# Optimization experiments

Measured on AMD Instinct MI355X. Metric: run time of the kernel, lower is better.

Reference implementation:

```python
import jax, jax.numpy as jnp
import numpy as np

N_USERS = 100000
N_ITEMS = 200000
N_NODES = N_USERS + N_ITEMS
EMB_DIM = 64
N_EDGES = 4000000
N_LAYERS = 2
BATCH = 8192
EMB_REG = 2.5e-5


def setup_inputs() -> dict:
    key = jax.random.key(0)
    k = jax.random.split(key, 7)
    return {
        "user_emb": jax.random.normal(k[0], (N_USERS, EMB_DIM), jnp.float32) * 0.1,
        "item_emb": jax.random.normal(k[1], (N_ITEMS, EMB_DIM), jnp.float32) * 0.1,
        "all_h": jax.random.randint(k[2], (N_EDGES,), 0, N_NODES, jnp.int64 if jax.config.jax_enable_x64 else jnp.int32),
        "all_t": jax.random.randint(k[3], (N_EDGES,), 0, N_NODES, jnp.int64 if jax.config.jax_enable_x64 else jnp.int32),
        "users": jax.random.randint(k[4], (BATCH,), 0, N_USERS),
        "pos_items": jax.random.randint(k[5], (BATCH,), 0, N_ITEMS),
        "neg_items": jax.random.randint(k[6], (BATCH,), 0, N_ITEMS),
    }


def _spmm(h, t, vals, x):
    # out[h] += vals * x[t]  over all edges; [N_NODES, D]
    return jax.ops.segment_sum(vals[:, None] * x[t], h, num_segments=N_NODES)


def reference(user_emb, item_emb, all_h, all_t, users, pos_items, neg_items):
    # symmetric normalization G = D^{-1/2} A D^{-1/2} on the edge list
    deg = jax.ops.segment_sum(jnp.ones((all_h.shape[0],), user_emb.dtype), all_h,
                              num_segments=N_NODES)
    dinv = jnp.where(deg > 0, deg ** -0.5, 0.0)
    g_vals = dinv[all_h] * dinv[all_t]

    # inference1: n_layers of SpMM with residual; sum over all layer outputs
    # (dropout p=0 on the main branch in the source -> identity)
    emb = jnp.concatenate([user_emb, item_emb], axis=0)  # [N, D]
    acc = emb
    for _ in range(N_LAYERS):
        emb = _spmm(all_h, all_t, g_vals, emb) + emb
        acc = acc + emb
    ua, ia = acc[:N_USERS], acc[N_USERS:]

    # BPR loss on the batch
    u = ua[users]
    pos = ia[pos_items]
    neg = ia[neg_items]
    pos_scores = jnp.sum(u * pos, axis=1)
    neg_scores = jnp.sum(u * neg, axis=1)
    mf_loss = jnp.mean(jax.nn.softplus(neg_scores - pos_scores))

    # embedding L2 regularization on the pre-propagation embeddings
    u_pre = user_emb[users]
    pos_pre = item_emb[pos_items]
    neg_pre = item_emb[neg_items]
    emb_loss = EMB_REG * (jnp.sum(u_pre ** 2) + jnp.sum(pos_pre ** 2)
                          + jnp.sum(neg_pre ** 2))
    return (mf_loss, emb_loss)
```

## Files before the change

### kernel.cpp

```cpp
#include <hip/hip_runtime.h>
#include <math.h>

#define N_USERS 100000
#define N_ITEMS 200000
#define N_NODES 300000
#define EMB_DIM 64
#define N_EDGES 4000000
#define BATCH   8192
#define EMB_REG 2.5e-05f

#define BUCK_SH 9
#define BN      512
#define NBUCK   586
#define BSLOT   7424
#define EPB     8192
#define EPT     32
#define NBLK_A  489
#define PACK_SH 19
#define SCORE_BLOCKS (BATCH / 4)
#define BLOCKS_PER_RANGE 9375

typedef unsigned short u16;
typedef unsigned int   u32;
typedef unsigned char  u8;
typedef __attribute__((ext_vector_type(8))) u16 u16x8;
typedef __attribute__((ext_vector_type(2))) float f32x2;

__device__ __forceinline__ float bf2f(u16 x) {
    u32 u = ((u32)x) << 16;
    return __builtin_bit_cast(float, u);
}
__device__ __forceinline__ u16 f2bf(float f) {
    u32 u = __builtin_bit_cast(u32, f);
    return (u16)((u + 0x7FFFu + ((u >> 16) & 1u)) >> 16);
}

__global__ void k_init(int* __restrict__ bcur) {
    int i = blockIdx.x * blockDim.x + threadIdx.x;
    if (i < NBUCK) bcur[i] = i * BSLOT;
}

__global__ void k_mark(const int* __restrict__ users, const int* __restrict__ pos,
                       const int* __restrict__ neg, u8* __restrict__ flags) {
    int i = blockIdx.x * blockDim.x + threadIdx.x;
    if (i < BATCH) {
        flags[users[i]] = 1;
        flags[N_USERS + pos[i]] = 1;
        flags[N_USERS + neg[i]] = 1;
    }
}

__global__ __launch_bounds__(256) void kA(const int* __restrict__ hh,
                                          const int* __restrict__ tt,
                                          int* __restrict__ bcur, int* __restrict__ gp) {
    __shared__ int sh_cnt[NBUCK];
    __shared__ int sh_base[NBUCK];
    int tid = threadIdx.x;
    for (int j = tid; j < NBUCK; j += 256) sh_cnt[j] = 0;
    __syncthreads();
    int cbase = blockIdx.x * EPB;
    int clen  = min(EPB, N_EDGES - cbase);
    int pk[EPT], bk[EPT];
    #pragma unroll
    for (int j = 0; j < EPT; ++j) {
        int i = j * 256 + tid;
        bk[j] = -1;
        if (i < clen) {
            int h = hh[cbase + i];
            int t = tt[cbase + i];
            int b = h >> BUCK_SH;
            bk[j] = b;
            pk[j] = ((h & (BN - 1)) << PACK_SH) | t;
            atomicAdd(&sh_cnt[b], 1);
        }
    }
    __syncthreads();
    for (int j = tid; j < NBUCK; j += 256) {
        int c = sh_cnt[j];
        sh_base[j] = c ? atomicAdd(&bcur[j], c) : 0;
        sh_cnt[j] = 0;
    }
    __syncthreads();
    #pragma unroll
    for (int j = 0; j < EPT; ++j) {
        if (bk[j] >= 0) {
            int r = atomicAdd(&sh_cnt[bk[j]], 1);
            gp[sh_base[bk[j]] + r] = pk[j];
        }
    }
}

__global__ __launch_bounds__(256) void kB(const int* __restrict__ bcur,
                                          int* __restrict__ gp,
                                          int2* __restrict__ sde, float* __restrict__ dinv,
                                          const float* __restrict__ uemb,
                                          const float* __restrict__ iemb,
                                          u8* __restrict__ e0s8) {
    __shared__ int   ncnt[BN];
    __shared__ int   noff[BN];
    __shared__ float sdv[BN];
    __shared__ int   slots[BSLOT];
    int b = blockIdx.x;
    int node0 = b << BUCK_SH;
    int nn = min(BN, N_NODES - node0);
    int base = b * BSLOT;
    int count = bcur[b] - base;
    int tid = threadIdx.x;
    for (int j = tid; j < BN; j += 256) ncnt[j] = 0;
    __syncthreads();
    for (int i = tid; i < count; i += 256)
        atomicAdd(&ncnt[gp[base + i] >> PACK_SH], 1);
    __syncthreads();
    if (tid < 64) {
        int lane = tid, carry = 0;
        #pragma unroll
        for (int b0 = 0; b0 < BN; b0 += 64) {
            int idx = b0 + lane;
            int v = ncnt[idx];
            int incl = v;
            #pragma unroll
            for (int d = 1; d < 64; d <<= 1) {
                int u = __shfl_up(incl, d, 64);
                if (lane >= d) incl += u;
            }
            noff[idx] = carry + incl - v;
            carry += __shfl(incl, 63, 64);
        }
    }
    __syncthreads();
    for (int j = tid; j < nn; j += 256) {
        int c = ncnt[j];
        float dv = c > 0 ? rsqrtf((float)c) : 0.0f;
        sde[node0 + j]  = make_int2(base + noff[j], c);
        dinv[node0 + j] = dv;
        sdv[j] = dv;
    }
    __syncthreads();
    for (int j = tid; j < BN; j += 256) ncnt[j] = noff[j];
    __syncthreads();
    for (int i = tid; i < count; i += 256) {
        int p = gp[base + i];
        int r = atomicAdd(&ncnt[p >> PACK_SH], 1);
        slots[r] = p & ((1 << PACK_SH) - 1);
    }
    __syncthreads();
    for (int i = tid; i < count; i += 256)
        gp[base + i] = slots[i];
    for (int i = tid; i < nn * 8; i += 256) {
        int j = i >> 3;
        float sc = sdv[j];
        int gnode = node0 + j;
        size_t ebase = (size_t)gnode * EMB_DIM + (size_t)(i & 7) * 8;
        const size_t UELEMS = (size_t)N_USERS * EMB_DIM;
        const float* src = (ebase < UELEMS) ? uemb + ebase : iemb + (ebase - UELEMS);
        float4 a  = ((const float4*)src)[0];
        float4 c4 = ((const float4*)src)[1];
        u32 w0 = __builtin_amdgcn_cvt_pk_fp8_f32(sc * a.x,  sc * a.y,  0,  false);
        w0 = __builtin_amdgcn_cvt_pk_fp8_f32(sc * a.z,  sc * a.w,  w0, true);
        u32 w1 = __builtin_amdgcn_cvt_pk_fp8_f32(sc * c4.x, sc * c4.y, 0,  false);
        w1 = __builtin_amdgcn_cvt_pk_fp8_f32(sc * c4.z, sc * c4.w, w1, true);
        uint2 o; o.x = w0; o.y = w1;
        ((uint2*)e0s8)[(size_t)gnode * 8 + (i & 7)] = o;
    }
}

__global__ void k_spmm1(const int2* __restrict__ sde,
                        const int* __restrict__ et,
                        const float* __restrict__ dinv,
                        const u8* __restrict__ src8,
                        const float* __restrict__ uemb, const float* __restrict__ iemb,
                        const u8* __restrict__ flags,
                        u16* __restrict__ dstb, u8* __restrict__ dst8) {
    int b = blockIdx.x;
    int node = ((b & 7) * BLOCKS_PER_RANGE + (b >> 3)) * 4 + (threadIdx.x >> 6);
    int lane = threadIdx.x & 63;
    int grp = lane >> 3;
    int sl  = lane & 7;
    int2 se = sde[node];
    int s = se.x, ne = se.y;
    float dh = dinv[node];
    int ets = (lane < ne) ? et[s + lane] : 0;
    float acc[8] = {0.f, 0.f, 0.f, 0.f, 0.f, 0.f, 0.f, 0.f};
    int lim = ne < 64 ? ne : 64;
    for (int j = grp; j < lim; j += 8) {
        int t = __shfl(ets, j, 64);
        uint2 d8 = ((const uint2*)(src8 + (size_t)t * EMB_DIM))[sl];
        f32x2 p0 = __builtin_amdgcn_cvt_pk_f32_fp8(d8.x, false);
        f32x2 p1 = __builtin_amdgcn_cvt_pk_f32_fp8(d8.x, true);
        f32x2 p2 = __builtin_amdgcn_cvt_pk_f32_fp8(d8.y, false);
        f32x2 p3 = __builtin_amdgcn_cvt_pk_f32_fp8(d8.y, true);
        acc[0] += p0.x; acc[1] += p0.y;
        acc[2] += p1.x; acc[3] += p1.y;
        acc[4] += p2.x; acc[5] += p2.y;
        acc[6] += p3.x; acc[7] += p3.y;
    }
    for (int i = s + 64 + grp; i < s + ne; i += 8) {
        int t = et[i];
        uint2 d8 = ((const uint2*)(src8 + (size_t)t * EMB_DIM))[sl];
        f32x2 p0 = __builtin_amdgcn_cvt_pk_f32_fp8(d8.x, false);
        f32x2 p1 = __builtin_amdgcn_cvt_pk_f32_fp8(d8.x, true);
        f32x2 p2 = __builtin_amdgcn_cvt_pk_f32_fp8(d8.y, false);
        f32x2 p3 = __builtin_amdgcn_cvt_pk_f32_fp8(d8.y, true);
        acc[0] += p0.x; acc[1] += p0.y;
        acc[2] += p1.x; acc[3] += p1.y;
        acc[4] += p2.x; acc[5] += p2.y;
        acc[6] += p3.x; acc[7] += p3.y;
    }
    #pragma unroll
    for (int m = 8; m <= 32; m <<= 1) {
        #pragma unroll
        for (int k = 0; k < 8; ++k)
            acc[k] += __shfl_xor(acc[k], m, 64);
    }
    if (grp == 0) {
        const float* srow = (node < N_USERS)
            ? uemb + (size_t)node * EMB_DIM
            : iemb + (size_t)(node - N_USERS) * EMB_DIM;
        float4 a = ((const float4*)srow)[sl * 2];
        float4 c = ((const float4*)srow)[sl * 2 + 1];
        float v[8];
        v[0] = dh * acc[0] + a.x; v[1] = dh * acc[1] + a.y;
        v[2] = dh * acc[2] + a.z; v[3] = dh * acc[3] + a.w;
        v[4] = dh * acc[4] + c.x; v[5] = dh * acc[5] + c.y;
        v[6] = dh * acc[6] + c.z; v[7] = dh * acc[7] + c.w;
        u32 w0 = __builtin_amdgcn_cvt_pk_fp8_f32(dh * v[0], dh * v[1], 0, false);
        w0 = __builtin_amdgcn_cvt_pk_fp8_f32(dh * v[2], dh * v[3], w0, true);
        u32 w1 = __builtin_amdgcn_cvt_pk_fp8_f32(dh * v[4], dh * v[5], 0, false);
        w1 = __builtin_amdgcn_cvt_pk_fp8_f32(dh * v[6], dh * v[7], w1, true);
        uint2 ow; ow.x = w0; ow.y = w1;
        ((uint2*)(dst8 + (size_t)node * EMB_DIM))[sl] = ow;
        if (flags[node]) {
            u16x8 o;
            o.s0 = f2bf(v[0]); o.s1 = f2bf(v[1]); o.s2 = f2bf(v[2]); o.s3 = f2bf(v[3]);
            o.s4 = f2bf(v[4]); o.s5 = f2bf(v[5]); o.s6 = f2bf(v[6]); o.s7 = f2bf(v[7]);
            ((u16x8*)(dstb + (size_t)node * EMB_DIM))[sl] = o;
        }
    }
}

__global__ void k_score(const int* __restrict__ users, const int* __restrict__ pos,
                        const int* __restrict__ neg,
                        const float* __restrict__ uemb, const float* __restrict__ iemb,
                        const u16* __restrict__ emb1b, const u8* __restrict__ emb1s8,
                        const int2* __restrict__ sde, const int* __restrict__ et,
                        const float* __restrict__ dinv,
                        float* __restrict__ pmf, float* __restrict__ psq) {
    __shared__ float smf[4], ssq[4];
    int gid = blockIdx.x * blockDim.x + threadIdx.x;
    int b = gid >> 6;
    int d = gid & 63;
    int w = threadIdx.x >> 6;
    int u  = users[b];
    int pi = pos[b];
    int ni = neg[b];
    int nodes[3];
    nodes[0] = u; nodes[1] = N_USERS + pi; nodes[2] = N_USERS + ni;
    float pre[3];
    pre[0] = uemb[(size_t)u * EMB_DIM + d];
    pre[1] = iemb[(size_t)pi * EMB_DIM + d];
    pre[2] = iemb[(size_t)ni * EMB_DIM + d];
    int s0[3], ne[3], ets[3];
    float dv[3];
    #pragma unroll
    for (int k = 0; k < 3; ++k) {
        int v = nodes[k];
        int2 se = sde[v];
        s0[k] = se.x; ne[k] = se.y;
        dv[k] = dinv[v];
        ets[k] = (d < ne[k]) ? et[se.x + d] : 0;
    }
    float a[3];
    #pragma unroll
    for (int k = 0; k < 3; ++k) {
        float ac = 0.f;
        int lim = ne[k] < 64 ? ne[k] : 64;
        for (int j = 0; j < lim; ++j) {
            int t = __shfl(ets[k], j, 64);
            u32 byte = emb1s8[(size_t)t * EMB_DIM + d];
            ac += __builtin_amdgcn_cvt_f32_fp8(byte, 0);
        }
        for (int i = s0[k] + 64; i < s0[k] + ne[k]; ++i) {
            int t = et[i];
            u32 byte = emb1s8[(size_t)t * EMB_DIM + d];
            ac += __builtin_amdgcn_cvt_f32_fp8(byte, 0);
        }
        a[k] = pre[k] + 2.0f * bf2f(emb1b[(size_t)nodes[k] * EMB_DIM + d]) + dv[k] * ac;
    }
    float ps = a[0] * a[1];
    float ns = a[0] * a[2];
    float sq = pre[0] * pre[0] + pre[1] * pre[1] + pre[2] * pre[2];
    #pragma unroll
    for (int off2 = 32; off2 > 0; off2 >>= 1) {
        ps += __shfl_down(ps, off2, 64);
        ns += __shfl_down(ns, off2, 64);
        sq += __shfl_down(sq, off2, 64);
    }
    if (d == 0) {
        float x  = ns - ps;
        smf[w] = fmaxf(x, 0.0f) + log1pf(expf(-fabsf(x)));
        ssq[w] = sq;
    }
    __syncthreads();
    if (threadIdx.x == 0) {
        pmf[blockIdx.x] = smf[0] + smf[1] + smf[2] + smf[3];
        psq[blockIdx.x] = ssq[0] + ssq[1] + ssq[2] + ssq[3];
    }
}

__global__ void k_final(const float* __restrict__ pmf, const float* __restrict__ psq,
                        float* __restrict__ out) {
    __shared__ float smf[4], ssq[4];
    int tid = threadIdx.x;
    float mf = 0.f, sq = 0.f;
    #pragma unroll
    for (int i = 0; i < SCORE_BLOCKS / 256; ++i) {
        mf += pmf[tid + i * 256];
        sq += psq[tid + i * 256];
    }
    #pragma unroll
    for (int off2 = 32; off2 > 0; off2 >>= 1) {
        mf += __shfl_down(mf, off2, 64);
        sq += __shfl_down(sq, off2, 64);
    }
    if ((tid & 63) == 0) { smf[tid >> 6] = mf; ssq[tid >> 6] = sq; }
    __syncthreads();
    if (tid == 0) {
        out[0] = (smf[0] + smf[1] + smf[2] + smf[3]) * (1.0f / BATCH);
        out[1] = EMB_REG * (ssq[0] + ssq[1] + ssq[2] + ssq[3]);
    }
}

extern "C" void kernel_launch(void* const* d_in, const int* in_sizes, int n_in,
                              void* d_out, int out_size, void* d_ws, size_t ws_size,
                              hipStream_t stream) {
    const float* uemb  = (const float*)d_in[0];
    const float* iemb  = (const float*)d_in[1];
    const int*   all_h = (const int*)d_in[2];
    const int*   all_t = (const int*)d_in[3];
    const int*   users = (const int*)d_in[4];
    const int*   pos   = (const int*)d_in[5];
    const int*   neg   = (const int*)d_in[6];
    float* out = (float*)d_out;

    int*   ws     = (int*)d_ws;
    float* dinv   = (float*)ws;
    int2*  sde    = (int2*)(ws + 300032);
    int*   bcur   = ws + 900096;
    u8*    flags  = (u8*)(ws + 901120);
    float* pmf    = (float*)(ws + 976128);
    float* psq    = (float*)(ws + 978176);
    int*   gp     = ws + 980224;
    u8*    e0s8   = (u8*)(ws + 5330688);
    u8*    emb1s8 = (u8*)(ws + 10130688);
    u16*   emb1b  = (u16*)(ws + 14930688);

    hipMemsetAsync(flags, 0, N_NODES, stream);

    k_init <<<3, 256, 0, stream>>>(bcur);
    k_mark <<<BATCH / 256, 256, 0, stream>>>(users, pos, neg, flags);
    kA     <<<NBLK_A, 256, 0, stream>>>(all_h, all_t, bcur, gp);
    kB     <<<NBUCK, 256, 0, stream>>>(bcur, gp, sde, dinv, uemb, iemb, e0s8);

    k_spmm1<<<N_NODES / 4, 256, 0, stream>>>(sde, gp, dinv, e0s8, uemb, iemb,
                                             flags, emb1b, emb1s8);

    k_score<<<SCORE_BLOCKS, 256, 0, stream>>>(users, pos, neg, uemb, iemb,
                                              emb1b, emb1s8, sde, gp, dinv, pmf, psq);
    k_final<<<1, 256, 0, stream>>>(pmf, psq, out);
}
```

Before: 340.9 us.

## Map one 8-lane group per node in SpMM and compute dinv inline

The first-layer SpMM kernel now assigns each node to an 8-lane subgroup (8 nodes per wavefront, 32 per block) instead of a full 64-lane wavefront, which removes the cross-lane shuffle reduction and avoids idle lanes on low-degree nodes. Edge indices are loaded 8 at a time per group and broadcast by shuffle, and the loop runs to the wave-wide maximum degree. The degree normalisation is recomputed as rsqrt of the edge count instead of being loaded from the dinv array. Divergence between nodes of different degree inside a wave can leave lanes idle, and the interleaved block-to-node mapping is dropped.

```diff
diff --git a/kernel.cpp b/kernel.cpp
--- a/kernel.cpp
+++ b/kernel.cpp
@@ -18,7 +18,6 @@
 #define NBLK_A  489
 #define PACK_SH 19
 #define SCORE_BLOCKS (BATCH / 4)
-#define BLOCKS_PER_RANGE 9375
 
 typedef unsigned short u16;
 typedef unsigned int   u32;
@@ -164,77 +163,65 @@
     }
 }
 
-__global__ void k_spmm1(const int2* __restrict__ sde,
+__global__ __launch_bounds__(256) void k_spmm1(const int2* __restrict__ sde,
                         const int* __restrict__ et,
-                        const float* __restrict__ dinv,
                         const u8* __restrict__ src8,
                         const float* __restrict__ uemb, const float* __restrict__ iemb,
                         const u8* __restrict__ flags,
                         u16* __restrict__ dstb, u8* __restrict__ dst8) {
-    int b = blockIdx.x;
-    int node = ((b & 7) * BLOCKS_PER_RANGE + (b >> 3)) * 4 + (threadIdx.x >> 6);
     int lane = threadIdx.x & 63;
-    int grp = lane >> 3;
-    int sl  = lane & 7;
+    int g    = lane >> 3;
+    int sl   = lane & 7;
+    int gb   = lane & 56;
+    int node = blockIdx.x * 32 + ((threadIdx.x >> 6) << 3) + g;
     int2 se = sde[node];
     int s = se.x, ne = se.y;
-    float dh = dinv[node];
-    int ets = (lane < ne) ? et[s + lane] : 0;
+    float dh = ne > 0 ? rsqrtf((float)ne) : 0.0f;
+    int mx = ne;
+    mx = max(mx, __shfl_xor(mx, 8, 64));
+    mx = max(mx, __shfl_xor(mx, 16, 64));
+    mx = max(mx, __shfl_xor(mx, 32, 64));
     float acc[8] = {0.f, 0.f, 0.f, 0.f, 0.f, 0.f, 0.f, 0.f};
-    int lim = ne < 64 ? ne : 64;
-    for (int j = grp; j < lim; j += 8) {
-        int t = __shfl(ets, j, 64);
-        uint2 d8 = ((const uint2*)(src8 + (size_t)t * EMB_DIM))[sl];
-        f32x2 p0 = __builtin_amdgcn_cvt_pk_f32_fp8(d8.x, false);
-        f32x2 p1 = __builtin_amdgcn_cvt_pk_f32_fp8(d8.x, true);
-        f32x2 p2 = __builtin_amdgcn_cvt_pk_f32_fp8(d8.y, false);
-        f32x2 p3 = __builtin_amdgcn_cvt_pk_f32_fp8(d8.y, true);
-        acc[0] += p0.x; acc[1] += p0.y;
-        acc[2] += p1.x; acc[3] += p1.y;
-        acc[4] += p2.x; acc[5] += p2.y;
-        acc[6] += p3.x; acc[7] += p3.y;
-    }
-    for (int i = s + 64 + grp; i < s + ne; i += 8) {
-        int t = et[i];
-        uint2 d8 = ((const uint2*)(src8 + (size_t)t * EMB_DIM))[sl];
-        f32x2 p0 = __builtin_amdgcn_cvt_pk_f32_fp8(d8.x, false);
-        f32x2 p1 = __builtin_amdgcn_cvt_pk_f32_fp8(d8.x, true);
-        f32x2 p2 = __builtin_amdgcn_cvt_pk_f32_fp8(d8.y, false);
-        f32x2 p3 = __builtin_amdgcn_cvt_pk_f32_fp8(d8.y, true);
-        acc[0] += p0.x; acc[1] += p0.y;
-        acc[2] += p1.x; acc[3] += p1.y;
-        acc[4] += p2.x; acc[5] += p2.y;
-        acc[6] += p3.x; acc[7] += p3.y;
-    }
-    #pragma unroll
-    for (int m = 8; m <= 32; m <<= 1) {
+    for (int j0 = 0; j0 < mx; j0 += 8) {
+        int idx = j0 + sl;
+        int ets = (idx < ne) ? et[s + idx] : 0;
         #pragma unroll
-        for (int k = 0; k < 8; ++k)
-            acc[k] += __shfl_xor(acc[k], m, 64);
-    }
-    if (grp == 0) {
-        const float* srow = (node < N_USERS)
-            ? uemb + (size_t)node * EMB_DIM
-            : iemb + (size_t)(node - N_USERS) * EMB_DIM;
-        float4 a = ((const float4*)srow)[sl * 2];
-        float4 c = ((const float4*)srow)[sl * 2 + 1];
-        float v[8];
-        v[0] = dh * acc[0] + a.x; v[1] = dh * acc[1] + a.y;
-        v[2] = dh * acc[2] + a.z; v[3] = dh * acc[3] + a.w;
-        v[4] = dh * acc[4] + c.x; v[5] = dh * acc[5] + c.y;
-        v[6] = dh * acc[6] + c.z; v[7] = dh * acc[7] + c.w;
-        u32 w0 = __builtin_amdgcn_cvt_pk_fp8_f32(dh * v[0], dh * v[1], 0, false);
-        w0 = __builtin_amdgcn_cvt_pk_fp8_f32(dh * v[2], dh * v[3], w0, true);
-        u32 w1 = __builtin_amdgcn_cvt_pk_fp8_f32(dh * v[4], dh * v[5], 0, false);
-        w1 = __builtin_amdgcn_cvt_pk_fp8_f32(dh * v[6], dh * v[7], w1, true);
-        uint2 ow; ow.x = w0; ow.y = w1;
-        ((uint2*)(dst8 + (size_t)node * EMB_DIM))[sl] = ow;
-        if (flags[node]) {
-            u16x8 o;
-            o.s0 = f2bf(v[0]); o.s1 = f2bf(v[1]); o.s2 = f2bf(v[2]); o.s3 = f2bf(v[3]);
-            o.s4 = f2bf(v[4]); o.s5 = f2bf(v[5]); o.s6 = f2bf(v[6]); o.s7 = f2bf(v[7]);
-            ((u16x8*)(dstb + (size_t)node * EMB_DIM))[sl] = o;
-        }
+        for (int jj = 0; jj < 8; ++jj) {
+            if (j0 + jj < ne) {
+                int t = __shfl(ets, gb | jj, 64);
+                uint2 d8 = ((const uint2*)(src8 + (size_t)t * EMB_DIM))[sl];
+                f32x2 p0 = __builtin_amdgcn_cvt_pk_f32_fp8(d8.x, false);
+                f32x2 p1 = __builtin_amdgcn_cvt_pk_f32_fp8(d8.x, true);
+                f32x2 p2 = __builtin_amdgcn_cvt_pk_f32_fp8(d8.y, false);
+                f32x2 p3 = __builtin_amdgcn_cvt_pk_f32_fp8(d8.y, true);
+                acc[0] += p0.x; acc[1] += p0.y;
+                acc[2] += p1.x; acc[3] += p1.y;
+                acc[4] += p2.x; acc[5] += p2.y;
+                acc[6] += p3.x; acc[7] += p3.y;
+            }
+        }
+    }
+    const float* srow = (node < N_USERS)
+        ? uemb + (size_t)node * EMB_DIM
+        : iemb + (size_t)(node - N_USERS) * EMB_DIM;
+    float4 a = ((const float4*)srow)[sl * 2];
+    float4 c = ((const float4*)srow)[sl * 2 + 1];
+    float v[8];
+    v[0] = dh * acc[0] + a.x; v[1] = dh * acc[1] + a.y;
+    v[2] = dh * acc[2] + a.z; v[3] = dh * acc[3] + a.w;
+    v[4] = dh * acc[4] + c.x; v[5] = dh * acc[5] + c.y;
+    v[6] = dh * acc[6] + c.z; v[7] = dh * acc[7] + c.w;
+    u32 w0 = __builtin_amdgcn_cvt_pk_fp8_f32(dh * v[0], dh * v[1], 0, false);
+    w0 = __builtin_amdgcn_cvt_pk_fp8_f32(dh * v[2], dh * v[3], w0, true);
+    u32 w1 = __builtin_amdgcn_cvt_pk_fp8_f32(dh * v[4], dh * v[5], 0, false);
+    w1 = __builtin_amdgcn_cvt_pk_fp8_f32(dh * v[6], dh * v[7], w1, true);
+    uint2 ow; ow.x = w0; ow.y = w1;
+    ((uint2*)(dst8 + (size_t)node * EMB_DIM))[sl] = ow;
+    if (flags[node]) {
+        u16x8 o;
+        o.s0 = f2bf(v[0]); o.s1 = f2bf(v[1]); o.s2 = f2bf(v[2]); o.s3 = f2bf(v[3]);
+        o.s4 = f2bf(v[4]); o.s5 = f2bf(v[5]); o.s6 = f2bf(v[6]); o.s7 = f2bf(v[7]);
+        ((u16x8*)(dstb + (size_t)node * EMB_DIM))[sl] = o;
     }
 }
 
@@ -361,8 +348,8 @@
     kA     <<<NBLK_A, 256, 0, stream>>>(all_h, all_t, bcur, gp);
     kB     <<<NBUCK, 256, 0, stream>>>(bcur, gp, sde, dinv, uemb, iemb, e0s8);
 
-    k_spmm1<<<N_NODES / 4, 256, 0, stream>>>(sde, gp, dinv, e0s8, uemb, iemb,
-                                             flags, emb1b, emb1s8);
+    k_spmm1<<<N_NODES / 32, 256, 0, stream>>>(sde, gp, e0s8, uemb, iemb,
+                                              flags, emb1b, emb1s8);
 
     k_score<<<SCORE_BLOCKS, 256, 0, stream>>>(users, pos, neg, uemb, iemb,
                                               emb1b, emb1s8, sde, gp, dinv, pmf, psq);
```

Result: faster. 304.0 us (-10.8%).
